# Performance work log

Hardware: AMD Instinct MI355X
Metric: run time of the kernel (lower is better)

## Reference

```python
import jax, jax.numpy as jnp
import numpy as np

B, NPG, C = 256, 256, 256  # graphs, nodes-per-graph, in_channels
MAX_LEN = 500


def _sinusoid_pe(max_len, c):
    pos = np.arange(max_len, dtype=np.float32)[:, None]
    div = np.exp(np.arange(0, c, 2, dtype=np.float32) * (-np.log(10000.0) / c))
    pe = np.zeros((max_len, c), np.float32)
    pe[:, 0::2] = np.sin(pos * div)
    pe[:, 1::2] = np.cos(pos * div)
    return jnp.asarray(pe)


def setup_inputs() -> dict:
    key = jax.random.key(0)
    ks = jax.random.split(key, 8)
    N = B * NPG
    x = jax.random.normal(ks[0], (N, C), jnp.float32)
    batch = jnp.repeat(jnp.arange(B, dtype=jnp.int32), NPG)
    # every other atom in each graph is an N/O atom -> 128 per graph
    on_index = (jnp.arange(B, dtype=jnp.int32)[:, None] * NPG
                + jnp.arange(0, NPG, 2, dtype=jnp.int32)[None, :]).reshape(-1)
    W1 = jax.random.normal(ks[1], (C, 256), jnp.float32) / np.sqrt(C)
    b1 = jnp.zeros((256,), jnp.float32)
    W2 = jax.random.normal(ks[2], (256, 128), jnp.float32) / np.sqrt(256.0)
    b2 = jnp.zeros((128,), jnp.float32)
    W3 = jax.random.normal(ks[3], (128, 64), jnp.float32) / np.sqrt(128.0)
    b3 = jnp.zeros((64,), jnp.float32)
    w_atom = jax.random.normal(ks[4], (64,), jnp.float32) / 8.0
    return {"x": x, "pe": _sinusoid_pe(MAX_LEN, C), "W1": W1, "b1": b1,
            "W2": W2, "b2": b2, "W3": W3, "b3": b3, "w_atom": w_atom,
            "batch": batch, "on_index": on_index, "ratio": 16}


def _lrelu(z):
    return jnp.where(z > 0, z, 0.1 * z)


def reference(x, pe, W1, b1, W2, b2, W3, b3, w_atom, batch, on_index, ratio):
    N = x.shape[0]
    bsz = int(batch[-1]) + 1
    num_nodes = jax.ops.segment_sum(jnp.ones_like(batch), batch, num_segments=bsz)
    cum = jnp.concatenate([jnp.zeros((1,), batch.dtype), jnp.cumsum(num_nodes)[:-1]])
    n = int(num_nodes.max())  # max_num_nodes
    idx_in_graph = jnp.arange(N, dtype=batch.dtype) - cum[batch]
    # positional encoding (dropout = identity in eval)
    xp = x + pe[idx_in_graph]
    # scoring MLP
    h = _lrelu(xp @ W1 + b1)
    h = _lrelu(h @ W2 + b2)
    h = _lrelu(h @ W3 + b3)
    score = jnp.tanh((h * w_atom).sum(-1) / jnp.linalg.norm(w_atom))
    # dense-pack scores into [bsz, n] padded with -inf, sort descending per row
    dense_idx = jnp.arange(N, dtype=batch.dtype) - cum[batch] + batch * n
    dense = jnp.full((bsz * n,), jnp.finfo(x.dtype).min, x.dtype).at[dense_idx].set(score)
    order = jnp.argsort(-dense.reshape(bsz, n), axis=-1)       # perm within row
    ranks = jnp.argsort(order, axis=-1)                         # inverse perm
    pos_in_perm = (jnp.arange(bsz)[:, None] * n + ranks).reshape(-1)
    # positions (in the flattened perm) of N/O atoms, sorted -> grouped per graph
    on_par = dense_idx[on_index]                                # padded/parallel ids
    indices = jnp.sort(pos_in_perm[on_par])
    m = on_index.shape[0] // bsz                                # N/O atoms per graph (uniform here)
    k = min(int(ratio), m)                                      # k = min(ratio, on_num)
    pre_mask = (jnp.arange(bsz)[:, None] * m + jnp.arange(k)[None, :]).reshape(-1)
    mask = indices[pre_mask]
    # map padded indices back to global node ids (subtract cumulative void counts)
    void = n - num_nodes
    cum_void = jnp.concatenate([jnp.zeros((1,), batch.dtype), jnp.cumsum(void)[:-1]])
    perm_flat = (order + (jnp.arange(bsz) * n - cum_void)[:, None]).reshape(-1)
    perm = perm_flat[mask]
    x_top = (xp[perm] * score[perm][:, None]).reshape(bsz, int(ratio), -1)
    return (x_top, perm, score[on_index], on_index)
```

## Files before the change

### kernel.cpp

```cpp
#include <hip/hip_runtime.h>
#include <hip/hip_bf16.h>


typedef __attribute__((ext_vector_type(8))) short short8v;
typedef __attribute__((ext_vector_type(4))) float float4v;

#define W1P_OFF 0
#define W2P_OFF 131072
#define W3P_OFF 196608
#define SCORES_OFF 212992

static __device__ __forceinline__ float lrelu(float z) { return z > 0.0f ? z : 0.1f * z; }

static __device__ __forceinline__ short f2bf(float f) {
    union { float f; unsigned u; } v; v.f = f;
    const unsigned r = v.u + 0x7FFFu + ((v.u >> 16) & 1u);
    return (short)(r >> 16);
}

static __device__ __forceinline__ int sw_off(int row, int chunk, int within) {
    return row * 256 + ((chunk ^ (row & 7)) << 3) + within;
}

__global__ __launch_bounds__(256) void pack_kernel(
    const float* __restrict__ W1, const float* __restrict__ W2,
    const float* __restrict__ W3, short* __restrict__ ws)
{
    const int u = blockIdx.x * 256 + threadIdx.x;
    if (u >= 13312) return;
    const float* W; int N, unitBase, uu;
    short* dst;
    if (u < 8192)       { W = W1; N = 256; uu = u;         dst = ws + (W1P_OFF/2); unitBase = 8; }
    else if (u < 12288) { W = W2; N = 128; uu = u - 8192;  dst = ws + (W2P_OFF/2); unitBase = 8; }
    else                { W = W3; N = 64;  uu = u - 12288; dst = ws + (W3P_OFF/2); unitBase = 4; }
    const int perNt = unitBase * 64;
    const int nt   = uu / perNt;
    const int rem  = uu % perNt;
    const int ks   = rem / 64;
    const int lane = rem % 64;
    const int q = lane >> 4;
    const int n = nt * 16 + (lane & 15);
    short8v frag;
    #pragma unroll
    for (int j = 0; j < 8; ++j) {
        const int k = ks * 32 + q * 8 + j;
        frag[j] = f2bf(W[(size_t)k * N + n]);
    }
    *(short8v*)(dst + (size_t)uu * 8) = frag;
}

__global__ __launch_bounds__(512, 4) void mlp_score_kernel(
    const float* __restrict__ x, const float* __restrict__ pe,
    const float* __restrict__ b1, const float* __restrict__ b2,
    const float* __restrict__ b3, const float* __restrict__ w_atom,
    const int* __restrict__ on_index, const short* __restrict__ ws_pack,
    float* __restrict__ ws_scores,
    float* __restrict__ out_score, float* __restrict__ out_onidx)
{
    __shared__ __align__(16) short XP[64 * 256];
    __shared__ __align__(16) short H1[64 * 256];
    const int t   = threadIdx.x;
    const int m0  = blockIdx.x * 64;
    const int wid = t >> 6;
    const int lane = t & 63;
    const int q = lane >> 4;
    const int c = lane & 15;

    const short* W1p = ws_pack + (W1P_OFF / 2);
    const short* W2p = ws_pack + (W2P_OFF / 2);
    const short* W3p = ws_pack + (W3P_OFF / 2);

    #pragma unroll
    for (int i = 0; i < 4; ++i) {
        const int u = t + i * 512;
        const int r = u >> 5;
        const int ck = u & 31;
        const int k = ck << 3;
        const int node = on_index[m0 + r];
        const float4 xa = *(const float4*)(x + (size_t)node * 256 + k);
        const float4 xb = *(const float4*)(x + (size_t)node * 256 + k + 4);
        const float4 pa = *(const float4*)(pe + (size_t)(node & 255) * 256 + k);
        const float4 pb = *(const float4*)(pe + (size_t)(node & 255) * 256 + k + 4);
        short8v s;
        s[0] = f2bf(xa.x + pa.x); s[1] = f2bf(xa.y + pa.y);
        s[2] = f2bf(xa.z + pa.z); s[3] = f2bf(xa.w + pa.w);
        s[4] = f2bf(xb.x + pb.x); s[5] = f2bf(xb.y + pb.y);
        s[6] = f2bf(xb.z + pb.z); s[7] = f2bf(xb.w + pb.w);
        *(short8v*)(&XP[sw_off(r, ck, 0)]) = s;
    }
    __syncthreads();

    #pragma unroll
    for (int g = 0; g < 2; ++g) {
        const int nt = wid * 2 + g;
        float4v acc[4];
        const float bb = b1[nt * 16 + c];
        #pragma unroll
        for (int mt = 0; mt < 4; ++mt) acc[mt] = (float4v){bb, bb, bb, bb};
        #pragma unroll
        for (int ks = 0; ks < 8; ++ks) {
            const short8v b = *(const short8v*)(W1p + ((size_t)(nt * 8 + ks) * 64 + lane) * 8);
            #pragma unroll
            for (int mt = 0; mt < 4; ++mt) {
                const short8v a = *(const short8v*)(&XP[sw_off(mt * 16 + c, ks * 4 + q, 0)]);
                acc[mt] = __builtin_amdgcn_mfma_f32_16x16x32_bf16(a, b, acc[mt], 0, 0, 0);
            }
        }
        #pragma unroll
        for (int mt = 0; mt < 4; ++mt)
            #pragma unroll
            for (int r = 0; r < 4; ++r) {
                const int row = mt * 16 + q * 4 + r;
                const int col = nt * 16 + c;
                H1[sw_off(row, col >> 3, col & 7)] = f2bf(lrelu(acc[mt][r]));
            }
    }
    __syncthreads();

    {
        const int nt = wid;
        float4v acc[4];
        const float bb = b2[nt * 16 + c];
        #pragma unroll
        for (int mt = 0; mt < 4; ++mt) acc[mt] = (float4v){bb, bb, bb, bb};
        #pragma unroll
        for (int ks = 0; ks < 8; ++ks) {
            const short8v b = *(const short8v*)(W2p + ((size_t)(nt * 8 + ks) * 64 + lane) * 8);
            #pragma unroll
            for (int mt = 0; mt < 4; ++mt) {
                const short8v a = *(const short8v*)(&H1[sw_off(mt * 16 + c, ks * 4 + q, 0)]);
                acc[mt] = __builtin_amdgcn_mfma_f32_16x16x32_bf16(a, b, acc[mt], 0, 0, 0);
            }
        }
        #pragma unroll
        for (int mt = 0; mt < 4; ++mt)
            #pragma unroll
            for (int r = 0; r < 4; ++r) {
                const int row = mt * 16 + q * 4 + r;
                const int col = nt * 16 + c;
                XP[sw_off(row, col >> 3, col & 7)] = f2bf(lrelu(acc[mt][r]));
            }
    }
    __syncthreads();

    {
        const int nt  = wid & 3;
        const int mt0 = (wid >> 2) * 2;
        float4v acc[2];
        const float bb = b3[nt * 16 + c];
        acc[0] = (float4v){bb, bb, bb, bb};
        acc[1] = (float4v){bb, bb, bb, bb};
        #pragma unroll
        for (int ks = 0; ks < 4; ++ks) {
            const short8v b = *(const short8v*)(W3p + ((size_t)(nt * 4 + ks) * 64 + lane) * 8);
            const short8v a0 = *(const short8v*)(&XP[sw_off((mt0 + 0) * 16 + c, ks * 4 + q, 0)]);
            const short8v a1 = *(const short8v*)(&XP[sw_off((mt0 + 1) * 16 + c, ks * 4 + q, 0)]);
            acc[0] = __builtin_amdgcn_mfma_f32_16x16x32_bf16(a0, b, acc[0], 0, 0, 0);
            acc[1] = __builtin_amdgcn_mfma_f32_16x16x32_bf16(a1, b, acc[1], 0, 0, 0);
        }
        float* H3F = (float*)H1;
        #pragma unroll
        for (int mt = 0; mt < 2; ++mt)
            #pragma unroll
            for (int r = 0; r < 4; ++r)
                H3F[((mt0 + mt) * 16 + q * 4 + r) * 68 + nt * 16 + c] = lrelu(acc[mt][r]);
    }
    __syncthreads();

    {
        const float* H3F = (const float*)H1;
        float* PART = (float*)XP;
        const int r = t >> 3, p = t & 7;
        float s = 0.0f;
        #pragma unroll
        for (int j = 0; j < 8; ++j) s += H3F[r * 68 + p * 8 + j] * w_atom[p * 8 + j];
        PART[t] = s;
        __syncthreads();
        if (t < 64) {
            float sum = 0.0f;
            #pragma unroll
            for (int pp = 0; pp < 8; ++pp) sum += PART[t * 8 + pp];
            float n2 = 0.0f;
            for (int cc = 0; cc < 64; ++cc) { const float w = w_atom[cc]; n2 += w * w; }
            const float sc = tanhf(sum / sqrtf(n2));
            const int m = m0 + t;
            ws_scores[m] = sc;
            out_score[m] = sc;
            out_onidx[m] = (float)on_index[m];
        }
    }
}

__global__ __launch_bounds__(256) void topk_gather_kernel(
    const float* __restrict__ x, const float* __restrict__ pe,
    const float* __restrict__ ws_scores, const int* __restrict__ on_index,
    float* __restrict__ out_perm, float* __restrict__ out_xtop)
{
    __shared__ float s[128];
    __shared__ int   sel_node[16];
    __shared__ float sel_sc[16];
    const int g = blockIdx.x, t = threadIdx.x;
    if (t < 128) s[t] = ws_scores[g * 128 + t];
    __syncthreads();
    if (t < 128) {
        const float sj = s[t];
        int rank = 0;
        for (int i = 0; i < 128; ++i) {
            const float si = s[i];
            rank += (si > sj) || (si == sj && i < t);
        }
        if (rank < 16) {
            const int node = on_index[g * 128 + t];
            sel_node[rank] = node;
            sel_sc[rank]   = sj;
            out_perm[g * 16 + rank] = (float)node;
        }
    }
    __syncthreads();
    #pragma unroll
    for (int k = 0; k < 16; ++k) {
        const int node = sel_node[k];
        const float sc = sel_sc[k];
        const float v = (x[(size_t)node * 256 + t] + pe[(size_t)(node & 255) * 256 + t]) * sc;
        out_xtop[((size_t)(g * 16 + k)) * 256 + t] = v;
    }
}

extern "C" void kernel_launch(void* const* d_in, const int* in_sizes, int n_in,
                              void* d_out, int out_size, void* d_ws, size_t ws_size,
                              hipStream_t stream)
{
    const float* x   = (const float*)d_in[0];
    const float* pe  = (const float*)d_in[1];
    const float* W1  = (const float*)d_in[2];
    const float* b1  = (const float*)d_in[3];
    const float* W2  = (const float*)d_in[4];
    const float* b2  = (const float*)d_in[5];
    const float* W3  = (const float*)d_in[6];
    const float* b3  = (const float*)d_in[7];
    const float* wa  = (const float*)d_in[8];
    const int* on_index = (const int*)d_in[10];

    float* out = (float*)d_out;
    float* out_xtop  = out;
    float* out_perm  = out + 1048576;
    float* out_score = out + 1048576 + 4096;
    float* out_onidx = out + 1048576 + 4096 + 32768;

    short* ws_pack   = (short*)d_ws;
    float* ws_scores = (float*)((char*)d_ws + SCORES_OFF);

    hipLaunchKernelGGL(pack_kernel, dim3(52), dim3(256), 0, stream, W1, W2, W3, ws_pack);
    hipLaunchKernelGGL(mlp_score_kernel, dim3(512), dim3(512), 0, stream,
                       x, pe, b1, b2, b3, wa, on_index, (const short*)ws_pack,
                       ws_scores, out_score, out_onidx);
    hipLaunchKernelGGL(topk_gather_kernel, dim3(256), dim3(256), 0, stream,
                       x, pe, ws_scores, on_index, out_perm, out_xtop);
}
```

Measured before the change: 128.6 us.

## Fuse MLP scoring and per-graph top-k gather into one kernel

Merges the scoring MLP and the top-k/gather kernels so each 1024-thread block handles one whole graph (128 N/O atoms). Scores stay in shared memory instead of making a global round trip, and one kernel launch is removed. In exchange, LDS per block doubles to about 128KB and the grid shrinks to 256 large blocks, which lowers occupancy and latency hiding.

```diff
diff --git a/kernel.cpp b/kernel.cpp
--- a/kernel.cpp
+++ b/kernel.cpp
@@ -8,7 +8,6 @@
 #define W1P_OFF 0
 #define W2P_OFF 131072
 #define W3P_OFF 196608
-#define SCORES_OFF 212992
 
 static __device__ __forceinline__ float lrelu(float z) { return z > 0.0f ? z : 0.1f * z; }
 
@@ -49,19 +48,24 @@
     *(short8v*)(dst + (size_t)uu * 8) = frag;
 }
 
-__global__ __launch_bounds__(512, 4) void mlp_score_kernel(
+__global__ __launch_bounds__(1024, 4) void fused_mlp_topk_kernel(
     const float* __restrict__ x, const float* __restrict__ pe,
     const float* __restrict__ b1, const float* __restrict__ b2,
     const float* __restrict__ b3, const float* __restrict__ w_atom,
     const int* __restrict__ on_index, const short* __restrict__ ws_pack,
-    float* __restrict__ ws_scores,
+    float* __restrict__ out_perm, float* __restrict__ out_xtop,
     float* __restrict__ out_score, float* __restrict__ out_onidx)
 {
-    __shared__ __align__(16) short XP[64 * 256];
-    __shared__ __align__(16) short H1[64 * 256];
-    const int t   = threadIdx.x;
-    const int m0  = blockIdx.x * 64;
-    const int wid = t >> 6;
+    __shared__ __align__(16) short XP[128 * 256];
+    __shared__ __align__(16) short H1[128 * 256];
+    __shared__ float SC[128];
+    __shared__ int   sel_node[16];
+    __shared__ float sel_sc[16];
+
+    const int t    = threadIdx.x;
+    const int g    = blockIdx.x;
+    const int m0   = g * 128;
+    const int wid  = t >> 6;
     const int lane = t & 63;
     const int q = lane >> 4;
     const int c = lane & 15;
@@ -72,7 +76,7 @@
 
     #pragma unroll
     for (int i = 0; i < 4; ++i) {
-        const int u = t + i * 512;
+        const int u = t + i * 1024;
         const int r = u >> 5;
         const int ck = u & 31;
         const int k = ck << 3;
@@ -90,24 +94,23 @@
     }
     __syncthreads();
 
-    #pragma unroll
-    for (int g = 0; g < 2; ++g) {
-        const int nt = wid * 2 + g;
-        float4v acc[4];
+    {
+        const int nt = wid;
+        float4v acc[8];
         const float bb = b1[nt * 16 + c];
         #pragma unroll
-        for (int mt = 0; mt < 4; ++mt) acc[mt] = (float4v){bb, bb, bb, bb};
+        for (int mt = 0; mt < 8; ++mt) acc[mt] = (float4v){bb, bb, bb, bb};
         #pragma unroll
         for (int ks = 0; ks < 8; ++ks) {
             const short8v b = *(const short8v*)(W1p + ((size_t)(nt * 8 + ks) * 64 + lane) * 8);
             #pragma unroll
-            for (int mt = 0; mt < 4; ++mt) {
+            for (int mt = 0; mt < 8; ++mt) {
                 const short8v a = *(const short8v*)(&XP[sw_off(mt * 16 + c, ks * 4 + q, 0)]);
                 acc[mt] = __builtin_amdgcn_mfma_f32_16x16x32_bf16(a, b, acc[mt], 0, 0, 0);
             }
         }
         #pragma unroll
-        for (int mt = 0; mt < 4; ++mt)
+        for (int mt = 0; mt < 8; ++mt)
             #pragma unroll
             for (int r = 0; r < 4; ++r) {
                 const int row = mt * 16 + q * 4 + r;
@@ -118,7 +121,8 @@
     __syncthreads();
 
     {
-        const int nt = wid;
+        const int nt  = wid & 7;
+        const int mt0 = (wid >> 3) * 4;
         float4v acc[4];
         const float bb = b2[nt * 16 + c];
         #pragma unroll
@@ -128,7 +132,7 @@
             const short8v b = *(const short8v*)(W2p + ((size_t)(nt * 8 + ks) * 64 + lane) * 8);
             #pragma unroll
             for (int mt = 0; mt < 4; ++mt) {
-                const short8v a = *(const short8v*)(&H1[sw_off(mt * 16 + c, ks * 4 + q, 0)]);
+                const short8v a = *(const short8v*)(&H1[sw_off((mt0 + mt) * 16 + c, ks * 4 + q, 0)]);
                 acc[mt] = __builtin_amdgcn_mfma_f32_16x16x32_bf16(a, b, acc[mt], 0, 0, 0);
             }
         }
@@ -136,7 +140,7 @@
         for (int mt = 0; mt < 4; ++mt)
             #pragma unroll
             for (int r = 0; r < 4; ++r) {
-                const int row = mt * 16 + q * 4 + r;
+                const int row = (mt0 + mt) * 16 + q * 4 + r;
                 const int col = nt * 16 + c;
                 XP[sw_off(row, col >> 3, col & 7)] = f2bf(lrelu(acc[mt][r]));
             }
@@ -176,53 +180,45 @@
         for (int j = 0; j < 8; ++j) s += H3F[r * 68 + p * 8 + j] * w_atom[p * 8 + j];
         PART[t] = s;
         __syncthreads();
-        if (t < 64) {
+        if (t < 128) {
             float sum = 0.0f;
             #pragma unroll
             for (int pp = 0; pp < 8; ++pp) sum += PART[t * 8 + pp];
             float n2 = 0.0f;
             for (int cc = 0; cc < 64; ++cc) { const float w = w_atom[cc]; n2 += w * w; }
             const float sc = tanhf(sum / sqrtf(n2));
-            const int m = m0 + t;
-            ws_scores[m] = sc;
-            out_score[m] = sc;
-            out_onidx[m] = (float)on_index[m];
-        }
-    }
-}
-
-__global__ __launch_bounds__(256) void topk_gather_kernel(
-    const float* __restrict__ x, const float* __restrict__ pe,
-    const float* __restrict__ ws_scores, const int* __restrict__ on_index,
-    float* __restrict__ out_perm, float* __restrict__ out_xtop)
-{
-    __shared__ float s[128];
-    __shared__ int   sel_node[16];
-    __shared__ float sel_sc[16];
-    const int g = blockIdx.x, t = threadIdx.x;
-    if (t < 128) s[t] = ws_scores[g * 128 + t];
-    __syncthreads();
+            SC[t] = sc;
+            out_score[m0 + t] = sc;
+            out_onidx[m0 + t] = (float)on_index[m0 + t];
+        }
+    }
+    __syncthreads();
+
     if (t < 128) {
-        const float sj = s[t];
+        const float sj = SC[t];
         int rank = 0;
         for (int i = 0; i < 128; ++i) {
-            const float si = s[i];
+            const float si = SC[i];
             rank += (si > sj) || (si == sj && i < t);
         }
         if (rank < 16) {
-            const int node = on_index[g * 128 + t];
+            const int node = on_index[m0 + t];
             sel_node[rank] = node;
             sel_sc[rank]   = sj;
             out_perm[g * 16 + rank] = (float)node;
         }
     }
     __syncthreads();
+
     #pragma unroll
-    for (int k = 0; k < 16; ++k) {
+    for (int i = 0; i < 4; ++i) {
+        const int idx = t + i * 1024;
+        const int k   = idx >> 8;
+        const int col = idx & 255;
         const int node = sel_node[k];
         const float sc = sel_sc[k];
-        const float v = (x[(size_t)node * 256 + t] + pe[(size_t)(node & 255) * 256 + t]) * sc;
-        out_xtop[((size_t)(g * 16 + k)) * 256 + t] = v;
+        const float v = (x[(size_t)node * 256 + col] + pe[(size_t)(node & 255) * 256 + col]) * sc;
+        out_xtop[((size_t)(g * 16 + k)) * 256 + col] = v;
     }
 }
 
@@ -247,13 +243,10 @@
     float* out_score = out + 1048576 + 4096;
     float* out_onidx = out + 1048576 + 4096 + 32768;
 
-    short* ws_pack   = (short*)d_ws;
-    float* ws_scores = (float*)((char*)d_ws + SCORES_OFF);
+    short* ws_pack = (short*)d_ws;
 
     hipLaunchKernelGGL(pack_kernel, dim3(52), dim3(256), 0, stream, W1, W2, W3, ws_pack);
-    hipLaunchKernelGGL(mlp_score_kernel, dim3(512), dim3(512), 0, stream,
+    hipLaunchKernelGGL(fused_mlp_topk_kernel, dim3(256), dim3(1024), 0, stream,
                        x, pe, b1, b2, b3, wa, on_index, (const short*)ws_pack,
-                       ws_scores, out_score, out_onidx);
-    hipLaunchKernelGGL(topk_gather_kernel, dim3(256), dim3(256), 0, stream,
-                       x, pe, ws_scores, on_index, out_perm, out_xtop);
-}
+                       out_perm, out_xtop, out_score, out_onidx);
+}
```

New measurement: 128.2 us. No clear change (-0.3%).
